# Kernel optimization log

Hardware: AMD Instinct MI355X
Metric: run time of the kernel (lower is better)

The kernel has to match this reference:

```python
import jax, jax.numpy as jnp
import numpy as np

B, N, C = 8, 100000, 64  # replicas, atoms, constraints


def setup_inputs() -> dict:
    key = jax.random.key(0)
    k1, k2, k3 = jax.random.split(key, 3)
    mom = jax.random.normal(k1, (B, N, 3), dtype=jnp.float32)
    # masses strictly positive
    mas = jax.random.uniform(k2, (B, N), dtype=jnp.float32, minval=0.5, maxval=1.5)
    dtm = jnp.full((B,), 1e-3, dtype=jnp.float32)  # timestep per replica
    jac_con_pos = jax.random.normal(k3, (B, C, N, 3), dtype=jnp.float32) * 0.1
    bme_lmd_tmp = jnp.zeros((B, C), dtype=jnp.float32)
    return {"mom": mom, "mas": mas, "dtm": dtm,
            "jac_con_pos": jac_con_pos, "bme_lmd_tmp": bme_lmd_tmp}


def reference(mom, mas, dtm, jac_con_pos, bme_lmd_tmp):
    # RATTLE momentum projection. rattle_objective is linear in lmd:
    #   dot(lmd) = b - dtm * G @ lmd,  G = J M^-1 J^T,  b = J M^-1 p
    # so the torch Newton loop converges exactly in one step to
    #   lmd = solve(dtm * G, b).
    inv_mas = 1.0 / mas                                   # [B,N]
    wjac = jac_con_pos * inv_mas[:, None, :, None]        # J M^-1, [B,C,N,3]
    b = jnp.einsum('bcnd,bnd->bc', wjac, mom)             # [B,C]
    G = jnp.einsum('bcnd,bknd->bck', wjac, jac_con_pos)   # [B,C,C]
    A = dtm[:, None, None] * G                            # Newton Jacobian (negated)
    lmd = jnp.linalg.solve(A, b[:, :, None])[:, :, 0]     # [B,C]
    frc = -jnp.einsum('bc,bcnd->bnd', lmd, jac_con_pos)   # constraint force
    mom_out = mom + frc * dtm[:, None, None]
    return mom_out, bme_lmd_tmp + lmd
```

## Files before the change

kernel.cpp:

```cpp
#include <hip/hip_runtime.h>

#define B_ 8
#define N_ 100000
#define C_ 64
#define K_ 300000
#define K4_ (K_/4)
#define AP_BLK ((K4_ + 255)/256)

#define KB 128
#define TILES ((K_ + KB - 1)/KB)
#define P1B 128

typedef __attribute__((ext_vector_type(8))) short short8;
typedef __attribute__((ext_vector_type(4))) float f32x4;

__device__ __forceinline__ unsigned int f2bf(float x) {
    union { float f; unsigned int u; } v; v.f = x;
    unsigned int r = v.u + 0x7FFFu + ((v.u >> 16) & 1u);
    return r >> 16;
}

__global__ __launch_bounds__(256) void zero_kernel(float* __restrict__ p, int n) {
    int i = blockIdx.x*256 + threadIdx.x;
    if (i < n) p[i] = 0.0f;
}

__global__ __launch_bounds__(256) void pass1_mfma(
    const float* __restrict__ jac, const float* __restrict__ mom,
    const float* __restrict__ mas, float* __restrict__ Gws, float* __restrict__ bws)
{
    __shared__ __align__(16) unsigned short sbf[64*KB];
    __shared__ __align__(16) float w_s[KB];
    __shared__ __align__(16) float sm_s[KB];

    const int b    = blockIdx.x / P1B;
    const int blk  = blockIdx.x % P1B;
    const int tid  = threadIdx.x;
    const int lane = tid & 63;
    const int wv   = tid >> 6;
    const int g    = tid & 15;
    const int r0   = tid >> 4;
    const int lrow = lane & 15;
    const int lkg  = lane >> 4;

    const float* jacb = jac + (size_t)b * C_ * K_;
    const float* momb = mom + (size_t)b * K_;
    const float* masb = mas + (size_t)b * N_;

    f32x4 acc[4] = {{0.f,0.f,0.f,0.f},{0.f,0.f,0.f,0.f},{0.f,0.f,0.f,0.f},{0.f,0.f,0.f,0.f}};
    float bacc[4] = {0.f, 0.f, 0.f, 0.f};

    for (int tile = blk; tile < TILES; tile += P1B) {
        const int k0 = tile * KB;

        if (tid < KB) {
            int k = k0 + tid;
            float w = 0.f, sm = 0.f;
            if (k < K_) { w = rsqrtf(masb[k/3]); sm = momb[k] * w; }
            w_s[tid] = w; sm_s[tid] = sm;
        }
        __syncthreads();

        #pragma unroll
        for (int i = 0; i < 4; ++i) {
            const int r  = r0 + 16*i;
            const int kb = k0 + g*8;
            uint4 pk = make_uint4(0u, 0u, 0u, 0u);
            if (kb < K_) {
                const float4 a0 = *(const float4*)&jacb[(size_t)r*K_ + kb];
                const float4 a1 = *(const float4*)&jacb[(size_t)r*K_ + kb + 4];
                const float4 w0 = *(const float4*)&w_s[g*8];
                const float4 w1 = *(const float4*)&w_s[g*8 + 4];
                const float4 m0 = *(const float4*)&sm_s[g*8];
                const float4 m1 = *(const float4*)&sm_s[g*8 + 4];
                const float s0 = a0.x*w0.x, s1 = a0.y*w0.y, s2 = a0.z*w0.z, s3 = a0.w*w0.w;
                const float s4 = a1.x*w1.x, s5 = a1.y*w1.y, s6 = a1.z*w1.z, s7 = a1.w*w1.w;
                bacc[i] += s0*m0.x + s1*m0.y + s2*m0.z + s3*m0.w
                         + s4*m1.x + s5*m1.y + s6*m1.z + s7*m1.w;
                pk.x = (f2bf(s1) << 16) | f2bf(s0);
                pk.y = (f2bf(s3) << 16) | f2bf(s2);
                pk.z = (f2bf(s5) << 16) | f2bf(s4);
                pk.w = (f2bf(s7) << 16) | f2bf(s6);
            }
            *(uint4*)&sbf[r*KB + ((g ^ (r & 15)) * 8)] = pk;
        }
        __syncthreads();

        const int ra = wv*16 + lrow;
        #pragma unroll
        for (int q = 0; q < 4; ++q) {
            const int ga = (q*4 + lkg) ^ (ra & 15);
            const short8 af = *(const short8*)&sbf[ra*KB + ga*8];
            #pragma unroll
            for (int p = 0; p < 4; ++p) {
                const int rb = p*16 + lrow;
                const int gb = (q*4 + lkg) ^ (rb & 15);
                const short8 bf = *(const short8*)&sbf[rb*KB + gb*8];
                acc[p] = __builtin_amdgcn_mfma_f32_16x16x32_bf16(af, bf, acc[p], 0, 0, 0);
            }
        }
    }

    float* Gb = Gws + b*4096;
    #pragma unroll
    for (int p = 0; p < 4; ++p) {
        #pragma unroll
        for (int reg = 0; reg < 4; ++reg) {
            const int row = 16*wv + lkg*4 + reg;
            const int col = 16*p + lrow;
            atomicAdd(&Gb[row*64 + col], acc[p][reg]);
        }
    }
    #pragma unroll
    for (int i = 0; i < 4; ++i) {
        float v = bacc[i];
        v += __shfl_xor(v, 1);
        v += __shfl_xor(v, 2);
        v += __shfl_xor(v, 4);
        v += __shfl_xor(v, 8);
        if ((tid & 15) == 0) atomicAdd(&bws[b*64 + r0 + 16*i], v);
    }
}

__global__ __launch_bounds__(256) void solve_kernel(
    const float* __restrict__ Gws, const float* __restrict__ bws,
    const float* __restrict__ dtm, const float* __restrict__ bme,
    float* __restrict__ lmd_ws, float* __restrict__ out_lmd)
{
    __shared__ float A[64*65];
    __shared__ float lmd_s[64];
    const int b = blockIdx.x;
    const int tid = threadIdx.x;
    const float dt = dtm[b];
    const float* Gb = Gws + b*4096;

    for (int e = tid; e < 64*65; e += 256) {
        int j = e / 65, k = e % 65;
        A[e] = (k < 64) ? dt * Gb[j*64 + k] : bws[b*64 + j];
    }
    __syncthreads();

    const int row = tid & 63;
    const int cg  = tid >> 6;
    for (int i = 0; i < 64; i++) {
        float f = 0.0f;
        if (row > i) f = A[row*65 + i] / A[i*65 + i];
        int k0 = i + 1;
        k0 += (cg - k0) & 3;
        if (row > i) {
            for (int k = k0; k <= 64; k += 4)
                A[row*65 + k] -= f * A[i*65 + k];
        }
        __syncthreads();
    }

    for (int i = 63; i >= 0; i--) {
        if (tid == i) lmd_s[i] = A[i*65 + 64] / A[i*65 + i];
        __syncthreads();
        if (tid < i) A[tid*65 + 64] -= A[tid*65 + i] * lmd_s[i];
        __syncthreads();
    }

    if (tid < 64) {
        float l = lmd_s[tid];
        lmd_ws[b*64 + tid] = l;
        out_lmd[b*64 + tid] = bme[b*64 + tid] + l;
    }
}

__global__ __launch_bounds__(256) void apply_kernel(
    const float* __restrict__ jac, const float* __restrict__ mom,
    const float* __restrict__ dtm, const float* __restrict__ lmd_ws,
    float* __restrict__ out)
{
    __shared__ float ls[64];
    const int b   = blockIdx.x / AP_BLK;
    const int blk = blockIdx.x % AP_BLK;
    if (threadIdx.x < 64) ls[threadIdx.x] = lmd_ws[b*64 + threadIdx.x] * dtm[b];
    __syncthreads();
    const int k4 = blk*256 + threadIdx.x;
    if (k4 >= K4_) return;

    const float4* jb = (const float4*)(jac + (size_t)b * C_ * K_);
    float4 a = make_float4(0.f, 0.f, 0.f, 0.f);
    #pragma unroll 8
    for (int c = 0; c < 64; c++) {
        float4 v = jb[(size_t)c * K4_ + k4];
        float l = ls[c];
        a.x -= l*v.x; a.y -= l*v.y; a.z -= l*v.z; a.w -= l*v.w;
    }
    const float4 m = ((const float4*)(mom + (size_t)b * K_))[k4];
    float4 o;
    o.x = m.x + a.x; o.y = m.y + a.y; o.z = m.z + a.z; o.w = m.w + a.w;
    ((float4*)out)[(size_t)b * K4_ + k4] = o;
}

extern "C" void kernel_launch(void* const* d_in, const int* in_sizes, int n_in,
                              void* d_out, int out_size, void* d_ws, size_t ws_size,
                              hipStream_t stream) {
    const float* mom = (const float*)d_in[0];
    const float* mas = (const float*)d_in[1];
    const float* dtm = (const float*)d_in[2];
    const float* jac = (const float*)d_in[3];
    const float* bme = (const float*)d_in[4];
    float* out = (float*)d_out;

    float* Gws    = (float*)d_ws;
    float* bws    = Gws + B_*4096;
    float* lmd_ws = bws + B_*64;

    const int nzero = B_*4096 + B_*64;
    zero_kernel<<<(nzero + 255)/256, 256, 0, stream>>>(Gws, nzero);
    pass1_mfma<<<B_*P1B, 256, 0, stream>>>(jac, mom, mas, Gws, bws);
    solve_kernel<<<B_, 256, 0, stream>>>(Gws, bws, dtm, bme, lmd_ws, out + (size_t)B_*K_);
    apply_kernel<<<B_*AP_BLK, 256, 0, stream>>>(jac, mom, dtm, lmd_ws, out);
}
```

Measured before the change: 301.6 us.

## Precompute mass weights in prep kernel and give pass1 blocks contiguous tiles

A prep kernel now zeroes the accumulators and computes rsqrt(mass) and the scaled momentum into workspace arrays. The Gram pass reads these directly from global memory instead of building them in shared memory each tile, which removes one barrier and the per-tile mass gather. Each block also handles a contiguous range of tiles instead of a strided set, and the weight and momentum loads are hoisted out of the row loop. The cost is an extra kernel that writes and re-reads roughly two K-sized arrays per replica.

```diff
diff --git a/kernel.cpp b/kernel.cpp
--- a/kernel.cpp
+++ b/kernel.cpp
@@ -10,6 +10,8 @@
 #define KB 128
 #define TILES ((K_ + KB - 1)/KB)
 #define P1B 128
+#define P1Q (TILES/P1B)
+#define P1R (TILES%P1B)
 
 typedef __attribute__((ext_vector_type(8))) short short8;
 typedef __attribute__((ext_vector_type(4))) float f32x4;
@@ -20,18 +22,35 @@
     return r >> 16;
 }
 
-__global__ __launch_bounds__(256) void zero_kernel(float* __restrict__ p, int n) {
-    int i = blockIdx.x*256 + threadIdx.x;
-    if (i < n) p[i] = 0.0f;
+__global__ __launch_bounds__(256) void prep_kernel(
+    const float* __restrict__ mas, const float* __restrict__ mom,
+    float* __restrict__ wk, float* __restrict__ smom,
+    float* __restrict__ zbuf, int nzero)
+{
+    const int i = blockIdx.x*256 + threadIdx.x;
+    if (i < nzero) zbuf[i] = 0.0f;
+    if (i < B_*K4_) {
+        const int b  = i / K4_;
+        const int k4 = i - b*K4_;
+        const int k  = 4*k4;
+        const float* mb = mas + (size_t)b*N_;
+        float4 w;
+        w.x = rsqrtf(mb[(k+0)/3]);
+        w.y = rsqrtf(mb[(k+1)/3]);
+        w.z = rsqrtf(mb[(k+2)/3]);
+        w.w = rsqrtf(mb[(k+3)/3]);
+        const float4 p = ((const float4*)(mom + (size_t)b*K_))[k4];
+        float4 s; s.x = p.x*w.x; s.y = p.y*w.y; s.z = p.z*w.z; s.w = p.w*w.w;
+        ((float4*)(wk   + (size_t)b*K_))[k4] = w;
+        ((float4*)(smom + (size_t)b*K_))[k4] = s;
+    }
 }
 
 __global__ __launch_bounds__(256) void pass1_mfma(
-    const float* __restrict__ jac, const float* __restrict__ mom,
-    const float* __restrict__ mas, float* __restrict__ Gws, float* __restrict__ bws)
+    const float* __restrict__ jac, const float* __restrict__ wk,
+    const float* __restrict__ smom, float* __restrict__ Gws, float* __restrict__ bws)
 {
     __shared__ __align__(16) unsigned short sbf[64*KB];
-    __shared__ __align__(16) float w_s[KB];
-    __shared__ __align__(16) float sm_s[KB];
 
     const int b    = blockIdx.x / P1B;
     const int blk  = blockIdx.x % P1B;
@@ -43,46 +62,49 @@
     const int lrow = lane & 15;
     const int lkg  = lane >> 4;
 
-    const float* jacb = jac + (size_t)b * C_ * K_;
-    const float* momb = mom + (size_t)b * K_;
-    const float* masb = mas + (size_t)b * N_;
+    const float* jacb = jac  + (size_t)b * C_ * K_;
+    const float* wkb  = wk   + (size_t)b * K_;
+    const float* smb  = smom + (size_t)b * K_;
+
+    const int start = blk*P1Q + (blk < P1R ? blk : P1R);
+    const int cnt   = P1Q + (blk < P1R ? 1 : 0);
 
     f32x4 acc[4] = {{0.f,0.f,0.f,0.f},{0.f,0.f,0.f,0.f},{0.f,0.f,0.f,0.f},{0.f,0.f,0.f,0.f}};
     float bacc[4] = {0.f, 0.f, 0.f, 0.f};
 
-    for (int tile = blk; tile < TILES; tile += P1B) {
-        const int k0 = tile * KB;
-
-        if (tid < KB) {
-            int k = k0 + tid;
-            float w = 0.f, sm = 0.f;
-            if (k < K_) { w = rsqrtf(masb[k/3]); sm = momb[k] * w; }
-            w_s[tid] = w; sm_s[tid] = sm;
-        }
-        __syncthreads();
-
-        #pragma unroll
-        for (int i = 0; i < 4; ++i) {
-            const int r  = r0 + 16*i;
-            const int kb = k0 + g*8;
-            uint4 pk = make_uint4(0u, 0u, 0u, 0u);
-            if (kb < K_) {
+    for (int t = 0; t < cnt; ++t) {
+        const int k0 = (start + t) * KB;
+        const int kb = k0 + g*8;
+        __syncthreads();
+
+        if (kb < K_) {
+            const float4 w0 = *(const float4*)&wkb[kb];
+            const float4 w1 = *(const float4*)&wkb[kb + 4];
+            const float4 m0 = *(const float4*)&smb[kb];
+            const float4 m1 = *(const float4*)&smb[kb + 4];
+            #pragma unroll
+            for (int i = 0; i < 4; ++i) {
+                const int r = r0 + 16*i;
                 const float4 a0 = *(const float4*)&jacb[(size_t)r*K_ + kb];
                 const float4 a1 = *(const float4*)&jacb[(size_t)r*K_ + kb + 4];
-                const float4 w0 = *(const float4*)&w_s[g*8];
-                const float4 w1 = *(const float4*)&w_s[g*8 + 4];
-                const float4 m0 = *(const float4*)&sm_s[g*8];
-                const float4 m1 = *(const float4*)&sm_s[g*8 + 4];
                 const float s0 = a0.x*w0.x, s1 = a0.y*w0.y, s2 = a0.z*w0.z, s3 = a0.w*w0.w;
                 const float s4 = a1.x*w1.x, s5 = a1.y*w1.y, s6 = a1.z*w1.z, s7 = a1.w*w1.w;
                 bacc[i] += s0*m0.x + s1*m0.y + s2*m0.z + s3*m0.w
                          + s4*m1.x + s5*m1.y + s6*m1.z + s7*m1.w;
+                uint4 pk;
                 pk.x = (f2bf(s1) << 16) | f2bf(s0);
                 pk.y = (f2bf(s3) << 16) | f2bf(s2);
                 pk.z = (f2bf(s5) << 16) | f2bf(s4);
                 pk.w = (f2bf(s7) << 16) | f2bf(s6);
+                *(uint4*)&sbf[r*KB + ((g ^ (r & 15)) * 8)] = pk;
             }
-            *(uint4*)&sbf[r*KB + ((g ^ (r & 15)) * 8)] = pk;
+        } else {
+            const uint4 pk = make_uint4(0u,0u,0u,0u);
+            #pragma unroll
+            for (int i = 0; i < 4; ++i) {
+                const int r = r0 + 16*i;
+                *(uint4*)&sbf[r*KB + ((g ^ (r & 15)) * 8)] = pk;
+            }
         }
         __syncthreads();
 
@@ -208,10 +230,12 @@
     float* Gws    = (float*)d_ws;
     float* bws    = Gws + B_*4096;
     float* lmd_ws = bws + B_*64;
+    float* wk     = lmd_ws + B_*64;
+    float* smom   = wk + (size_t)B_*K_;
 
     const int nzero = B_*4096 + B_*64;
-    zero_kernel<<<(nzero + 255)/256, 256, 0, stream>>>(Gws, nzero);
-    pass1_mfma<<<B_*P1B, 256, 0, stream>>>(jac, mom, mas, Gws, bws);
+    prep_kernel<<<(B_*K4_ + 255)/256, 256, 0, stream>>>(mas, mom, wk, smom, Gws, nzero);
+    pass1_mfma<<<B_*P1B, 256, 0, stream>>>(jac, wk, smom, Gws, bws);
     solve_kernel<<<B_, 256, 0, stream>>>(Gws, bws, dtm, bme, lmd_ws, out + (size_t)B_*K_);
     apply_kernel<<<B_*AP_BLK, 256, 0, stream>>>(jac, mom, dtm, lmd_ws, out);
 }
```

After: 325.3 us. +7.9%, slower.

## Cache Jacobian as FP8 in pass1 and read it in the apply kernel

Applied to the files above, without the earlier changes.

During the Gram pass, each Jacobian tile is also converted to packed FP8 and written to a workspace copy. The apply kernel then reads that 1-byte copy instead of re-reading the fp32 Jacobian, which should cut its read traffic by about 4x. The cost is extra writes in pass1 and a loss of precision in the constraint force. FP8 with roughly 3 mantissa bits may break tolerance, though dtm*lambda is small.

```diff
diff --git a/kernel.cpp b/kernel.cpp
--- a/kernel.cpp
+++ b/kernel.cpp
@@ -13,6 +13,7 @@
 
 typedef __attribute__((ext_vector_type(8))) short short8;
 typedef __attribute__((ext_vector_type(4))) float f32x4;
+typedef __attribute__((ext_vector_type(2))) float f32x2;
 
 __device__ __forceinline__ unsigned int f2bf(float x) {
     union { float f; unsigned int u; } v; v.f = x;
@@ -27,7 +28,8 @@
 
 __global__ __launch_bounds__(256) void pass1_mfma(
     const float* __restrict__ jac, const float* __restrict__ mom,
-    const float* __restrict__ mas, float* __restrict__ Gws, float* __restrict__ bws)
+    const float* __restrict__ mas, float* __restrict__ Gws, float* __restrict__ bws,
+    unsigned char* __restrict__ J8)
 {
     __shared__ __align__(16) unsigned short sbf[64*KB];
     __shared__ __align__(16) float w_s[KB];
@@ -46,6 +48,7 @@
     const float* jacb = jac + (size_t)b * C_ * K_;
     const float* momb = mom + (size_t)b * K_;
     const float* masb = mas + (size_t)b * N_;
+    unsigned char* J8b = J8 + (size_t)b * C_ * K_;
 
     f32x4 acc[4] = {{0.f,0.f,0.f,0.f},{0.f,0.f,0.f,0.f},{0.f,0.f,0.f,0.f},{0.f,0.f,0.f,0.f}};
     float bacc[4] = {0.f, 0.f, 0.f, 0.f};
@@ -73,6 +76,15 @@
                 const float4 w1 = *(const float4*)&w_s[g*8 + 4];
                 const float4 m0 = *(const float4*)&sm_s[g*8];
                 const float4 m1 = *(const float4*)&sm_s[g*8 + 4];
+                uint2 j8;
+                {
+                    int lo = __builtin_amdgcn_cvt_pk_fp8_f32(a0.x, a0.y, 0, false);
+                    lo     = __builtin_amdgcn_cvt_pk_fp8_f32(a0.z, a0.w, lo, true);
+                    int hi = __builtin_amdgcn_cvt_pk_fp8_f32(a1.x, a1.y, 0, false);
+                    hi     = __builtin_amdgcn_cvt_pk_fp8_f32(a1.z, a1.w, hi, true);
+                    j8.x = (unsigned int)lo; j8.y = (unsigned int)hi;
+                }
+                *(uint2*)&J8b[(size_t)r*K_ + kb] = j8;
                 const float s0 = a0.x*w0.x, s1 = a0.y*w0.y, s2 = a0.z*w0.z, s3 = a0.w*w0.w;
                 const float s4 = a1.x*w1.x, s5 = a1.y*w1.y, s6 = a1.z*w1.z, s7 = a1.w*w1.w;
                 bacc[i] += s0*m0.x + s1*m0.y + s2*m0.z + s3*m0.w
@@ -168,8 +180,8 @@
     }
 }
 
-__global__ __launch_bounds__(256) void apply_kernel(
-    const float* __restrict__ jac, const float* __restrict__ mom,
+__global__ __launch_bounds__(256) void apply8_kernel(
+    const unsigned char* __restrict__ J8, const float* __restrict__ mom,
     const float* __restrict__ dtm, const float* __restrict__ lmd_ws,
     float* __restrict__ out)
 {
@@ -181,13 +193,15 @@
     const int k4 = blk*256 + threadIdx.x;
     if (k4 >= K4_) return;
 
-    const float4* jb = (const float4*)(jac + (size_t)b * C_ * K_);
+    const unsigned char* jb = J8 + (size_t)b * C_ * K_;
     float4 a = make_float4(0.f, 0.f, 0.f, 0.f);
     #pragma unroll 8
     for (int c = 0; c < 64; c++) {
-        float4 v = jb[(size_t)c * K4_ + k4];
-        float l = ls[c];
-        a.x -= l*v.x; a.y -= l*v.y; a.z -= l*v.z; a.w -= l*v.w;
+        const unsigned int u = *(const unsigned int*)&jb[(size_t)c * K_ + 4*k4];
+        const f32x2 f01 = __builtin_amdgcn_cvt_pk_f32_fp8(u, false);
+        const f32x2 f23 = __builtin_amdgcn_cvt_pk_f32_fp8(u, true);
+        const float l = ls[c];
+        a.x -= l*f01[0]; a.y -= l*f01[1]; a.z -= l*f23[0]; a.w -= l*f23[1];
     }
     const float4 m = ((const float4*)(mom + (size_t)b * K_))[k4];
     float4 o;
@@ -208,10 +222,11 @@
     float* Gws    = (float*)d_ws;
     float* bws    = Gws + B_*4096;
     float* lmd_ws = bws + B_*64;
+    unsigned char* J8 = (unsigned char*)(lmd_ws + B_*64);
 
     const int nzero = B_*4096 + B_*64;
     zero_kernel<<<(nzero + 255)/256, 256, 0, stream>>>(Gws, nzero);
-    pass1_mfma<<<B_*P1B, 256, 0, stream>>>(jac, mom, mas, Gws, bws);
+    pass1_mfma<<<B_*P1B, 256, 0, stream>>>(jac, mom, mas, Gws, bws, J8);
     solve_kernel<<<B_, 256, 0, stream>>>(Gws, bws, dtm, bme, lmd_ws, out + (size_t)B_*K_);
-    apply_kernel<<<B_*AP_BLK, 256, 0, stream>>>(jac, mom, dtm, lmd_ws, out);
-}
+    apply8_kernel<<<B_*AP_BLK, 256, 0, stream>>>(J8, mom, dtm, lmd_ws, out);
+}
```

After: 300.0 us, median of 2. About the same (-0.5%).

## Stage fp32 Jacobian tiles into LDS via direct global-to-LDS loads

Applied to the files above, without the earlier changes.

The pass1 Gram kernel now uses global_load_lds to copy raw fp32 Jacobian tiles straight into a swizzled shared buffer, bypassing registers. Mass scaling, the b-vector dot product and bf16 packing move into the MFMA loop and are applied to fragments read from LDS. The aim is to overlap and simplify global loads and drop the separate convert-and-store phase. In exchange, LDS use doubles, each B fragment is scaled and converted redundantly by every wave, and an extra barrier is added per tile.

```diff
diff --git a/kernel.cpp b/kernel.cpp
--- a/kernel.cpp
+++ b/kernel.cpp
@@ -29,7 +29,7 @@
     const float* __restrict__ jac, const float* __restrict__ mom,
     const float* __restrict__ mas, float* __restrict__ Gws, float* __restrict__ bws)
 {
-    __shared__ __align__(16) unsigned short sbf[64*KB];
+    __shared__ __align__(16) float sjac[64*KB];
     __shared__ __align__(16) float w_s[KB];
     __shared__ __align__(16) float sm_s[KB];
 
@@ -38,17 +38,17 @@
     const int tid  = threadIdx.x;
     const int lane = tid & 63;
     const int wv   = tid >> 6;
-    const int g    = tid & 15;
-    const int r0   = tid >> 4;
     const int lrow = lane & 15;
     const int lkg  = lane >> 4;
+    const int half = lane >> 5;
+    const int s31  = lane & 31;
 
     const float* jacb = jac + (size_t)b * C_ * K_;
     const float* momb = mom + (size_t)b * K_;
     const float* masb = mas + (size_t)b * N_;
 
     f32x4 acc[4] = {{0.f,0.f,0.f,0.f},{0.f,0.f,0.f,0.f},{0.f,0.f,0.f,0.f},{0.f,0.f,0.f,0.f}};
-    float bacc[4] = {0.f, 0.f, 0.f, 0.f};
+    float bacc = 0.f;
 
     for (int tile = blk; tile < TILES; tile += P1B) {
         const int k0 = tile * KB;
@@ -59,46 +59,57 @@
             if (k < K_) { w = rsqrtf(masb[k/3]); sm = momb[k] * w; }
             w_s[tid] = w; sm_s[tid] = sm;
         }
-        __syncthreads();
-
         #pragma unroll
-        for (int i = 0; i < 4; ++i) {
-            const int r  = r0 + 16*i;
-            const int kb = k0 + g*8;
-            uint4 pk = make_uint4(0u, 0u, 0u, 0u);
-            if (kb < K_) {
-                const float4 a0 = *(const float4*)&jacb[(size_t)r*K_ + kb];
-                const float4 a1 = *(const float4*)&jacb[(size_t)r*K_ + kb + 4];
-                const float4 w0 = *(const float4*)&w_s[g*8];
-                const float4 w1 = *(const float4*)&w_s[g*8 + 4];
-                const float4 m0 = *(const float4*)&sm_s[g*8];
-                const float4 m1 = *(const float4*)&sm_s[g*8 + 4];
-                const float s0 = a0.x*w0.x, s1 = a0.y*w0.y, s2 = a0.z*w0.z, s3 = a0.w*w0.w;
-                const float s4 = a1.x*w1.x, s5 = a1.y*w1.y, s6 = a1.z*w1.z, s7 = a1.w*w1.w;
-                bacc[i] += s0*m0.x + s1*m0.y + s2*m0.z + s3*m0.w
-                         + s4*m1.x + s5*m1.y + s6*m1.z + s7*m1.w;
-                pk.x = (f2bf(s1) << 16) | f2bf(s0);
-                pk.y = (f2bf(s3) << 16) | f2bf(s2);
-                pk.z = (f2bf(s5) << 16) | f2bf(s4);
-                pk.w = (f2bf(s7) << 16) | f2bf(s6);
-            }
-            *(uint4*)&sbf[r*KB + ((g ^ (r & 15)) * 8)] = pk;
+        for (int j = 0; j < 8; ++j) {
+            const int row  = wv*16 + j*2 + half;
+            const int gsrc = s31 ^ (row & 15);
+            int kk = k0 + gsrc*4;
+            kk = (kk > K_ - 4) ? (K_ - 4) : kk;
+            const float* gp = &jacb[(size_t)row*K_ + kk];
+            float* lp = &sjac[(wv*16 + j*2)*KB];
+            __builtin_amdgcn_global_load_lds(
+                (const __attribute__((address_space(1))) void*)gp,
+                (__attribute__((address_space(3))) void*)lp, 16, 0, 0);
         }
         __syncthreads();
 
         const int ra = wv*16 + lrow;
         #pragma unroll
         for (int q = 0; q < 4; ++q) {
-            const int ga = (q*4 + lkg) ^ (ra & 15);
-            const short8 af = *(const short8*)&sbf[ra*KB + ga*8];
+            const int G0 = q*8 + lkg*2;
+            const int s0 = G0 ^ lrow;
+            const int s1 = (G0 + 1) ^ lrow;
+            const float4 w0 = *(const float4*)&w_s[G0*4];
+            const float4 w1 = *(const float4*)&w_s[G0*4 + 4];
+            const float4 m0 = *(const float4*)&sm_s[G0*4];
+            const float4 m1 = *(const float4*)&sm_s[G0*4 + 4];
+            const float4 a0 = *(const float4*)&sjac[ra*KB + s0*4];
+            const float4 a1 = *(const float4*)&sjac[ra*KB + s1*4];
+            const float s0f = a0.x*w0.x, s1f = a0.y*w0.y, s2f = a0.z*w0.z, s3f = a0.w*w0.w;
+            const float s4f = a1.x*w1.x, s5f = a1.y*w1.y, s6f = a1.z*w1.z, s7f = a1.w*w1.w;
+            bacc += s0f*m0.x + s1f*m0.y + s2f*m0.z + s3f*m0.w
+                  + s4f*m1.x + s5f*m1.y + s6f*m1.z + s7f*m1.w;
+            short8 af;
+            ((unsigned int*)&af)[0] = (f2bf(s1f) << 16) | f2bf(s0f);
+            ((unsigned int*)&af)[1] = (f2bf(s3f) << 16) | f2bf(s2f);
+            ((unsigned int*)&af)[2] = (f2bf(s5f) << 16) | f2bf(s4f);
+            ((unsigned int*)&af)[3] = (f2bf(s7f) << 16) | f2bf(s6f);
             #pragma unroll
             for (int p = 0; p < 4; ++p) {
                 const int rb = p*16 + lrow;
-                const int gb = (q*4 + lkg) ^ (rb & 15);
-                const short8 bf = *(const short8*)&sbf[rb*KB + gb*8];
+                const float4 b0 = *(const float4*)&sjac[rb*KB + s0*4];
+                const float4 b1 = *(const float4*)&sjac[rb*KB + s1*4];
+                const float t0 = b0.x*w0.x, t1 = b0.y*w0.y, t2 = b0.z*w0.z, t3 = b0.w*w0.w;
+                const float t4 = b1.x*w1.x, t5 = b1.y*w1.y, t6 = b1.z*w1.z, t7 = b1.w*w1.w;
+                short8 bf;
+                ((unsigned int*)&bf)[0] = (f2bf(t1) << 16) | f2bf(t0);
+                ((unsigned int*)&bf)[1] = (f2bf(t3) << 16) | f2bf(t2);
+                ((unsigned int*)&bf)[2] = (f2bf(t5) << 16) | f2bf(t4);
+                ((unsigned int*)&bf)[3] = (f2bf(t7) << 16) | f2bf(t6);
                 acc[p] = __builtin_amdgcn_mfma_f32_16x16x32_bf16(af, bf, acc[p], 0, 0, 0);
             }
         }
+        __syncthreads();
     }
 
     float* Gb = Gws + b*4096;
@@ -111,15 +122,9 @@
             atomicAdd(&Gb[row*64 + col], acc[p][reg]);
         }
     }
-    #pragma unroll
-    for (int i = 0; i < 4; ++i) {
-        float v = bacc[i];
-        v += __shfl_xor(v, 1);
-        v += __shfl_xor(v, 2);
-        v += __shfl_xor(v, 4);
-        v += __shfl_xor(v, 8);
-        if ((tid & 15) == 0) atomicAdd(&bws[b*64 + r0 + 16*i], v);
-    }
+    bacc += __shfl_xor(bacc, 16);
+    bacc += __shfl_xor(bacc, 32);
+    if (lkg == 0) atomicAdd(&bws[b*64 + wv*16 + lrow], bacc);
 }
 
 __global__ __launch_bounds__(256) void solve_kernel(
```

Result: slower. 329.8 us (+9.3%).
